# Performance work log

Hardware: AMD Instinct MI355X
Metric: run time of the kernel (lower is better)

Reference implementation:

```python
import jax, jax.numpy as jnp
import numpy as np

# ---- structural constants (mirror e3nn SO3.tensor_productRs bookkeeping) ----
MUL = 2                      # multiplicity of every irrep in Rs_in / Rs_out
LS = [0, 1, 2]               # irrep orders present in Rs_in and Rs_out
L_MAX = 2                    # spherical-harmonics cutoff -> Y_dim = 9
N_BASIS, HIDDEN = 64, 64     # radial model sizes
R_MAX, GAMMA = 3.5, 4.0      # gaussian radial basis params


def _filter_paths():
    """One entry (l_filter) per (mul_out, mul_in, l_in, l_out, l_f) path."""
    paths = []
    for l_in in LS:
        for l_out in LS:
            for lf in range(abs(l_in - l_out), min(l_in + l_out, L_MAX) + 1):
                paths.extend([lf] * (MUL * MUL))  # mul_in * mul_out copies
    return paths  # len == n_path == 60


def _build_mix_matrices():
    """rf_mix[K, n_path]: broadcast each radial path weight over its 2l+1 components.
    ylm_mix[K, 9]: select Y_{l,m} for each filter component. Both 0/1, block sparse."""
    paths = _filter_paths()
    n_path = len(paths)
    K = sum(2 * l + 1 for l in paths)          # 204
    y_off = {0: 0, 1: 1, 2: 4}                 # offset of l-block inside Y (dim 9)
    rf = np.zeros((K, n_path), dtype=np.float32)
    ylm = np.zeros((K, 9), dtype=np.float32)
    k = 0
    for p, l in enumerate(paths):
        for m in range(2 * l + 1):
            rf[k, p] = 1.0
            ylm[k, y_off[l] + m] = 1.0
            k += 1
    return rf, ylm, n_path, K


def _sh_l012(n):
    """Real spherical harmonics l=0..2 on unit vectors n[Z,3] -> Y[9, Z]."""
    x, y, z = n[:, 0], n[:, 1], n[:, 2]
    c0 = 0.28209479177387814   # 1/(2 sqrt(pi))
    c1 = 0.4886025119029199    # sqrt(3/(4 pi))
    c2a = 1.0925484305920792   # sqrt(15/(4 pi))
    c2b = 0.31539156525252005  # sqrt(5/(16 pi))
    c2c = 0.5462742152960396   # sqrt(15/(16 pi))
    one = jnp.ones_like(x)
    return jnp.stack([
        c0 * one,
        c1 * y, c1 * z, c1 * x,
        c2a * x * y, c2a * y * z, c2b * (3.0 * z * z - 1.0), c2a * x * z,
        c2c * (x * x - y * y),
    ], axis=0)


def setup_inputs() -> dict:
    key = jax.random.key(0)
    k_r, k_cg, k_w1, k_w2 = jax.random.split(key, 4)
    Z = 65536
    D = MUL * sum(2 * l + 1 for l in LS)       # 18 (dim_in == dim_out)
    rf_np, ylm_np, n_path, K = _build_mix_matrices()
    r = 2.0 * jax.random.normal(k_r, (Z, 3), dtype=jnp.float32)
    cg = jax.random.normal(k_cg, (K, D, D), dtype=jnp.float32) / np.sqrt(K)
    W1 = jax.random.normal(k_w1, (N_BASIS, HIDDEN), dtype=jnp.float32) / np.sqrt(N_BASIS)
    b1 = jnp.zeros((HIDDEN,), dtype=jnp.float32)
    W2 = jax.random.normal(k_w2, (HIDDEN, n_path), dtype=jnp.float32) / np.sqrt(HIDDEN)
    b2 = jnp.zeros((n_path,), dtype=jnp.float32)
    return {"r": r, "W1": W1, "b1": b1, "W2": W2, "b2": b2,
            "cg": cg, "rf_mix": jnp.asarray(rf_np), "ylm_mix": jnp.asarray(ylm_np)}


def reference(r, W1, b1, W2, b2, cg, rf_mix, ylm_mix):
    radii = jnp.linalg.norm(r, axis=1)                    # [Z]
    n = r / (radii[:, None] + 1e-12)                      # unit directions
    Y = _sh_l012(n)                                       # [9, Z]  (sh returns [m, ...])
    centers = jnp.linspace(0.0, R_MAX, N_BASIS, dtype=jnp.float32)
    B = jnp.exp(-GAMMA * (radii[:, None] - centers) ** 2) # gaussian radial basis [Z, 64]
    R = jax.nn.relu(B @ W1 + b1) @ W2 + b2                # RadialModel -> [Z, n_path]
    Rm = jnp.einsum('kp,zp->zk', rf_mix, R)               # 'ij,zj->zi'
    Ym = jnp.einsum('ky,yz->zk', ylm_mix, Y)              # 'ij,jz->zi'
    # 'kij,zk,zk->zij' : fuse the two per-point vectors, then one GEMM over k
    kernel = jnp.einsum('kij,zk->zij', cg, Rm * Ym)       # [Z, 18, 18]
    return kernel
```

## Files before the change

### kernel.cpp

```cpp
#include <hip/hip_runtime.h>

#define NPATH 60
#define KDIM  204
#define NIJ   324
#define NTIL  21
#define HID   64

typedef short bf16x8 __attribute__((ext_vector_type(8)));
typedef float f32x4  __attribute__((ext_vector_type(4)));

__device__ __align__(16) unsigned short g_w1s[4096];
__device__ __align__(16) unsigned short g_w2s[4096];
__device__ __align__(16) unsigned short g_cgs[75264];
__device__ unsigned int  g_pyk[112];

__device__ inline unsigned short f2bf(float f) {
    unsigned int u = __builtin_bit_cast(unsigned int, f);
    u += 0x7fffu + ((u >> 16) & 1u);
    return (unsigned short)(u >> 16);
}
__device__ inline float bf2f(unsigned short h) {
    unsigned int u = ((unsigned int)h) << 16;
    return __builtin_bit_cast(float, u);
}

__global__ void prep_kernel(const float* __restrict__ W1, const float* __restrict__ W2,
                            const float* __restrict__ cg, const float* __restrict__ rf,
                            const float* __restrict__ ylm)
{
    int idx = blockIdx.x * 256 + threadIdx.x;
    if (idx < 4096) {
        int e = idx & 7, ln = (idx >> 3) & 63, nt = (idx >> 9) & 3, kc = idx >> 11;
        int k = kc * 32 + (ln >> 4) * 8 + e;
        int n = nt * 16 + (ln & 15);
        g_w1s[idx] = f2bf(W1[k * HID + n]);
    } else if (idx < 8192) {
        int j = idx - 4096;
        int e = j & 7, ln = (j >> 3) & 63, nt = (j >> 9) & 3, kc = j >> 11;
        int k = kc * 32 + (ln >> 4) * 8 + e;
        int n = nt * 16 + (ln & 15);
        g_w2s[j] = f2bf(n < NPATH ? W2[k * NPATH + n] : 0.0f);
    } else if (idx < 8192 + 75264) {
        int j = idx - 8192;
        int e = j & 7, ln = (j >> 3) & 63;
        int nt = (j >> 9) % NTIL;
        int kc = j / (512 * NTIL);
        int k = kc * 32 + (ln >> 4) * 8 + e;
        int n = nt * 16 + (ln & 15);
        g_cgs[j] = f2bf((k < KDIM && n < NIJ) ? cg[k * NIJ + n] : 0.0f);
    } else if (idx < 8192 + 75264 + 112) {
        int j = idx - (8192 + 75264);
        int k0 = 2 * j, k1 = 2 * j + 1;
        unsigned p0 = 0, y0 = 0, p1 = 0, y1 = 0;
        if (k0 < KDIM) {
            for (int q = 0; q < NPATH; q++) if (rf[k0 * NPATH + q] != 0.0f) p0 = q;
            for (int q = 0; q < 9; q++)     if (ylm[k0 * 9 + q]   != 0.0f) y0 = q;
            for (int q = 0; q < NPATH; q++) if (rf[k1 * NPATH + q] != 0.0f) p1 = q;
            for (int q = 0; q < 9; q++)     if (ylm[k1 * 9 + q]   != 0.0f) y1 = q;
        }
        g_pyk[j] = p0 | (y0 << 8) | (p1 << 16) | (y1 << 24);
    }
}

struct __align__(16) WaveMem {
    unsigned short Hw[16][88];
    unsigned short Rw[16][61];
    float          Yw[16][9];
};

__global__ __launch_bounds__(256) void fused_kernel(
    const float* __restrict__ r, const float* __restrict__ b1,
    const float* __restrict__ b2, float* __restrict__ out)
{
    __shared__ WaveMem wm[4];

    const int tid  = threadIdx.x;
    const int wv   = tid >> 6;
    const int lane = tid & 63;
    const int quad = lane >> 4;
    const int l16  = lane & 15;
    const int z0   = blockIdx.x * 64;
    WaveMem& W = wm[wv];

    const int zg = z0 + wv * 16 + l16;
    float x = r[zg * 3 + 0], y = r[zg * 3 + 1], zc = r[zg * 3 + 2];
    float rad = sqrtf(x * x + y * y + zc * zc);

    if (quad == 0) {
        float inv = 1.0f / (rad + 1e-12f);
        float nx = x * inv, ny = y * inv, nz = zc * inv;
        const float c0 = 0.28209479177387814f, c1 = 0.4886025119029199f;
        const float c2a = 1.0925484305920792f, c2b = 0.31539156525252005f, c2c = 0.5462742152960396f;
        W.Yw[l16][0] = c0;
        W.Yw[l16][1] = c1 * ny;
        W.Yw[l16][2] = c1 * nz;
        W.Yw[l16][3] = c1 * nx;
        W.Yw[l16][4] = c2a * nx * ny;
        W.Yw[l16][5] = c2a * ny * nz;
        W.Yw[l16][6] = c2b * (3.0f * nz * nz - 1.0f);
        W.Yw[l16][7] = c2a * nx * nz;
        W.Yw[l16][8] = c2c * (nx * nx - ny * ny);
    }

    union frag { bf16x8 v; unsigned int d[4]; };
    frag A0, A1;
    {
        const float step = 3.5f / 63.0f;
        const float NL2E = -5.770780163555852f;
        #pragma unroll
        for (int ii = 0; ii < 4; ii++) {
            int i0 = quad * 8 + 2 * ii;
            float d0 = rad - (float)i0 * step;
            float d1 = rad - (float)(i0 + 1) * step;
            A0.d[ii] = (unsigned)f2bf(__builtin_amdgcn_exp2f(d0 * d0 * NL2E))
                     | ((unsigned)f2bf(__builtin_amdgcn_exp2f(d1 * d1 * NL2E)) << 16);
            int i2 = 32 + i0;
            float e0 = rad - (float)i2 * step;
            float e1 = rad - (float)(i2 + 1) * step;
            A1.d[ii] = (unsigned)f2bf(__builtin_amdgcn_exp2f(e0 * e0 * NL2E))
                     | ((unsigned)f2bf(__builtin_amdgcn_exp2f(e1 * e1 * NL2E)) << 16);
        }
    }

    #pragma unroll
    for (int nt = 0; nt < 4; nt++) {
        bf16x8 bb0 = *(const bf16x8*)&g_w1s[((0 * 4 + nt) * 64 + lane) * 8];
        bf16x8 bb1 = *(const bf16x8*)&g_w1s[((1 * 4 + nt) * 64 + lane) * 8];
        f32x4 acc = {0.f, 0.f, 0.f, 0.f};
        acc = __builtin_amdgcn_mfma_f32_16x16x32_bf16(A0.v, bb0, acc, 0, 0, 0);
        acc = __builtin_amdgcn_mfma_f32_16x16x32_bf16(A1.v, bb1, acc, 0, 0, 0);
        int h = nt * 16 + l16;
        float bias = b1[h];
        #pragma unroll
        for (int rr = 0; rr < 4; rr++) {
            float v = acc[rr] + bias;
            v = v > 0.0f ? v : 0.0f;
            W.Hw[quad * 4 + rr][h] = f2bf(v);
        }
    }
    asm volatile("s_waitcnt lgkmcnt(0)" ::: "memory");
    __builtin_amdgcn_sched_barrier(0);

    {
        bf16x8 h0 = *(const bf16x8*)&W.Hw[l16][0 + quad * 8];
        bf16x8 h1 = *(const bf16x8*)&W.Hw[l16][32 + quad * 8];
        #pragma unroll
        for (int nt = 0; nt < 4; nt++) {
            bf16x8 bb0 = *(const bf16x8*)&g_w2s[((0 * 4 + nt) * 64 + lane) * 8];
            bf16x8 bb1 = *(const bf16x8*)&g_w2s[((1 * 4 + nt) * 64 + lane) * 8];
            f32x4 acc = {0.f, 0.f, 0.f, 0.f};
            acc = __builtin_amdgcn_mfma_f32_16x16x32_bf16(h0, bb0, acc, 0, 0, 0);
            acc = __builtin_amdgcn_mfma_f32_16x16x32_bf16(h1, bb1, acc, 0, 0, 0);
            int p = nt * 16 + l16;
            if (p < NPATH) {
                float bias = b2[p];
                #pragma unroll
                for (int rr = 0; rr < 4; rr++)
                    W.Rw[quad * 4 + rr][p] = f2bf(acc[rr] + bias);
            }
        }
    }
    asm volatile("s_waitcnt lgkmcnt(0)" ::: "memory");
    __builtin_amdgcn_sched_barrier(0);

    frag az[7];
    #pragma unroll
    for (int kc = 0; kc < 7; kc++) {
        #pragma unroll
        for (int ii = 0; ii < 4; ii++) {
            unsigned py = g_pyk[kc * 16 + quad * 4 + ii];
            float cA = bf2f(W.Rw[l16][py & 255])         * W.Yw[l16][(py >> 8) & 255];
            float cB = bf2f(W.Rw[l16][(py >> 16) & 255]) * W.Yw[l16][py >> 24];
            az[kc].d[ii] = (unsigned)f2bf(cA) | ((unsigned)f2bf(cB) << 16);
        }
    }

    const int obase = (z0 + wv * 16 + quad * 4) * NIJ + l16;
    #pragma unroll 3
    for (int nt = 0; nt < NTIL; nt++) {
        f32x4 acc = {0.f, 0.f, 0.f, 0.f};
        #pragma unroll
        for (int kc = 0; kc < 7; kc++) {
            bf16x8 bg = *(const bf16x8*)&g_cgs[((kc * NTIL + nt) * 64 + lane) * 8];
            acc = __builtin_amdgcn_mfma_f32_16x16x32_bf16(az[kc].v, bg, acc, 0, 0, 0);
        }
        int col = nt * 16 + l16;
        if (col < NIJ) {
            #pragma unroll
            for (int rr = 0; rr < 4; rr++)
                out[obase + rr * NIJ + nt * 16] = acc[rr];
        }
    }
}

extern "C" void kernel_launch(void* const* d_in, const int* in_sizes, int n_in,
                              void* d_out, int out_size, void* d_ws, size_t ws_size,
                              hipStream_t stream) {
    const float* r   = (const float*)d_in[0];
    const float* W1  = (const float*)d_in[1];
    const float* b1  = (const float*)d_in[2];
    const float* W2  = (const float*)d_in[3];
    const float* b2  = (const float*)d_in[4];
    const float* cg  = (const float*)d_in[5];
    const float* rf  = (const float*)d_in[6];
    const float* ylm = (const float*)d_in[7];
    float* out = (float*)d_out;

    const int Z = in_sizes[0] / 3;

    prep_kernel<<<327, 256, 0, stream>>>(W1, W2, cg, rf, ylm);
    fused_kernel<<<Z / 64, 256, 0, stream>>>(r, b1, b2, out);
}
```

Measured before the change: 127.2 us.

## Process two 16-point tiles per wave to reuse CG fragments across MFMAs

Each wave now handles 32 points, running the radial MLP and coefficient phases twice into two A-fragment sets. In the final GEMM each loaded CG B-fragment feeds two MFMAs, halving CG loads per output and doubling the work per block (half as many blocks). The prep kernel's CG repack is also rewritten to iterate over source order so reads of cg are coalesced. The cost is more registers (two 7-fragment sets) and fewer blocks, which may reduce occupancy and latency hiding on the write-bound output stage.

```diff
diff --git a/kernel.cpp b/kernel.cpp
--- a/kernel.cpp
+++ b/kernel.cpp
@@ -42,12 +42,13 @@
         g_w2s[j] = f2bf(n < NPATH ? W2[k * NPATH + n] : 0.0f);
     } else if (idx < 8192 + 75264) {
         int j = idx - 8192;
-        int e = j & 7, ln = (j >> 3) & 63;
-        int nt = (j >> 9) % NTIL;
-        int kc = j / (512 * NTIL);
-        int k = kc * 32 + (ln >> 4) * 8 + e;
-        int n = nt * 16 + (ln & 15);
-        g_cgs[j] = f2bf((k < KDIM && n < NIJ) ? cg[k * NIJ + n] : 0.0f);
+        int k = j / 336;
+        int n = j % 336;
+        int kc = k >> 5, km = k & 31;
+        int e  = km & 7, lh = km >> 3;
+        int nt = n >> 4, lw = n & 15;
+        int dst = ((kc * NTIL + nt) * 64 + (lh * 16 + lw)) * 8 + e;
+        g_cgs[dst] = f2bf((k < KDIM && n < NIJ) ? cg[k * NIJ + n] : 0.0f);
     } else if (idx < 8192 + 75264 + 112) {
         int j = idx - (8192 + 75264);
         int k0 = 2 * j, k1 = 2 * j + 1;
@@ -68,6 +69,8 @@
     float          Yw[16][9];
 };
 
+union frag { bf16x8 v; unsigned int d[4]; };
+
 __global__ __launch_bounds__(256) void fused_kernel(
     const float* __restrict__ r, const float* __restrict__ b1,
     const float* __restrict__ b2, float* __restrict__ out)
@@ -79,116 +82,125 @@
     const int lane = tid & 63;
     const int quad = lane >> 4;
     const int l16  = lane & 15;
-    const int z0   = blockIdx.x * 64;
+    const int z0   = blockIdx.x * 128;
     WaveMem& W = wm[wv];
 
-    const int zg = z0 + wv * 16 + l16;
-    float x = r[zg * 3 + 0], y = r[zg * 3 + 1], zc = r[zg * 3 + 2];
-    float rad = sqrtf(x * x + y * y + zc * zc);
-
-    if (quad == 0) {
-        float inv = 1.0f / (rad + 1e-12f);
-        float nx = x * inv, ny = y * inv, nz = zc * inv;
-        const float c0 = 0.28209479177387814f, c1 = 0.4886025119029199f;
-        const float c2a = 1.0925484305920792f, c2b = 0.31539156525252005f, c2c = 0.5462742152960396f;
-        W.Yw[l16][0] = c0;
-        W.Yw[l16][1] = c1 * ny;
-        W.Yw[l16][2] = c1 * nz;
-        W.Yw[l16][3] = c1 * nx;
-        W.Yw[l16][4] = c2a * nx * ny;
-        W.Yw[l16][5] = c2a * ny * nz;
-        W.Yw[l16][6] = c2b * (3.0f * nz * nz - 1.0f);
-        W.Yw[l16][7] = c2a * nx * nz;
-        W.Yw[l16][8] = c2c * (nx * nx - ny * ny);
+    frag az0[7], az1[7];
+
+#define PHASES_AD(AZ, ZBASE)                                                          \
+    {                                                                                 \
+        const int zg = (ZBASE) + l16;                                                 \
+        float x = r[zg * 3 + 0], y = r[zg * 3 + 1], zc = r[zg * 3 + 2];               \
+        float rad = sqrtf(x * x + y * y + zc * zc);                                   \
+        if (quad == 0) {                                                              \
+            float inv = 1.0f / (rad + 1e-12f);                                        \
+            float nx = x * inv, ny = y * inv, nz = zc * inv;                          \
+            const float c0 = 0.28209479177387814f, c1 = 0.4886025119029199f;          \
+            const float c2a = 1.0925484305920792f, c2b = 0.31539156525252005f,        \
+                        c2c = 0.5462742152960396f;                                    \
+            W.Yw[l16][0] = c0;                                                        \
+            W.Yw[l16][1] = c1 * ny;                                                   \
+            W.Yw[l16][2] = c1 * nz;                                                   \
+            W.Yw[l16][3] = c1 * nx;                                                   \
+            W.Yw[l16][4] = c2a * nx * ny;                                             \
+            W.Yw[l16][5] = c2a * ny * nz;                                             \
+            W.Yw[l16][6] = c2b * (3.0f * nz * nz - 1.0f);                             \
+            W.Yw[l16][7] = c2a * nx * nz;                                             \
+            W.Yw[l16][8] = c2c * (nx * nx - ny * ny);                                 \
+        }                                                                             \
+        frag A0, A1;                                                                  \
+        {                                                                             \
+            const float step = 3.5f / 63.0f;                                          \
+            const float NL2E = -5.770780163555852f;                 \
+            _Pragma("unroll")                                                         \
+            for (int ii = 0; ii < 4; ii++) {                                          \
+                int i0 = quad * 8 + 2 * ii;                                           \
+                float d0 = rad - (float)i0 * step;                                    \
+                float d1 = rad - (float)(i0 + 1) * step;                              \
+                A0.d[ii] = (unsigned)f2bf(__builtin_amdgcn_exp2f(d0 * d0 * NL2E))     \
+                         | ((unsigned)f2bf(__builtin_amdgcn_exp2f(d1 * d1 * NL2E)) << 16); \
+                int i2 = 32 + i0;                                                     \
+                float e0 = rad - (float)i2 * step;                                    \
+                float e1 = rad - (float)(i2 + 1) * step;                              \
+                A1.d[ii] = (unsigned)f2bf(__builtin_amdgcn_exp2f(e0 * e0 * NL2E))     \
+                         | ((unsigned)f2bf(__builtin_amdgcn_exp2f(e1 * e1 * NL2E)) << 16); \
+            }                                                                         \
+        }                                                                             \
+        _Pragma("unroll")                                                             \
+        for (int nt = 0; nt < 4; nt++) {                                              \
+            bf16x8 bb0 = *(const bf16x8*)&g_w1s[((0 * 4 + nt) * 64 + lane) * 8];      \
+            bf16x8 bb1 = *(const bf16x8*)&g_w1s[((1 * 4 + nt) * 64 + lane) * 8];      \
+            f32x4 acc = {0.f, 0.f, 0.f, 0.f};                                         \
+            acc = __builtin_amdgcn_mfma_f32_16x16x32_bf16(A0.v, bb0, acc, 0, 0, 0);   \
+            acc = __builtin_amdgcn_mfma_f32_16x16x32_bf16(A1.v, bb1, acc, 0, 0, 0);   \
+            int h = nt * 16 + l16;                                                    \
+            float bias = b1[h];                                                       \
+            _Pragma("unroll")                                                         \
+            for (int rr = 0; rr < 4; rr++) {                                          \
+                float v = acc[rr] + bias;                                             \
+                v = v > 0.0f ? v : 0.0f;                                              \
+                W.Hw[quad * 4 + rr][h] = f2bf(v);                                     \
+            }                                                                         \
+        }                                                                             \
+        asm volatile("s_waitcnt lgkmcnt(0)" ::: "memory");                            \
+        __builtin_amdgcn_sched_barrier(0);                                            \
+        {                                                                             \
+            bf16x8 h0 = *(const bf16x8*)&W.Hw[l16][0 + quad * 8];                     \
+            bf16x8 h1 = *(const bf16x8*)&W.Hw[l16][32 + quad * 8];                    \
+            _Pragma("unroll")                                                         \
+            for (int nt = 0; nt < 4; nt++) {                                          \
+                bf16x8 bb0 = *(const bf16x8*)&g_w2s[((0 * 4 + nt) * 64 + lane) * 8];  \
+                bf16x8 bb1 = *(const bf16x8*)&g_w2s[((1 * 4 + nt) * 64 + lane) * 8];  \
+                f32x4 acc = {0.f, 0.f, 0.f, 0.f};                                     \
+                acc = __builtin_amdgcn_mfma_f32_16x16x32_bf16(h0, bb0, acc, 0, 0, 0); \
+                acc = __builtin_amdgcn_mfma_f32_16x16x32_bf16(h1, bb1, acc, 0, 0, 0); \
+                int p = nt * 16 + l16;                                                \
+                if (p < NPATH) {                                                      \
+                    float bias = b2[p];                                               \
+                    _Pragma("unroll")                                                 \
+                    for (int rr = 0; rr < 4; rr++)                                    \
+                        W.Rw[quad * 4 + rr][p] = f2bf(acc[rr] + bias);                \
+                }                                                                     \
+            }                                                                         \
+        }                                                                             \
+        asm volatile("s_waitcnt lgkmcnt(0)" ::: "memory");                            \
+        __builtin_amdgcn_sched_barrier(0);                                            \
+        _Pragma("unroll")                                                             \
+        for (int kc = 0; kc < 7; kc++) {                                              \
+            _Pragma("unroll")                                                         \
+            for (int ii = 0; ii < 4; ii++) {                                          \
+                unsigned py = g_pyk[kc * 16 + quad * 4 + ii];                         \
+                float cA = bf2f(W.Rw[l16][py & 255])         * W.Yw[l16][(py >> 8) & 255]; \
+                float cB = bf2f(W.Rw[l16][(py >> 16) & 255]) * W.Yw[l16][py >> 24];   \
+                AZ[kc].d[ii] = (unsigned)f2bf(cA) | ((unsigned)f2bf(cB) << 16);       \
+            }                                                                         \
+        }                                                                             \
+        asm volatile("s_waitcnt lgkmcnt(0)" ::: "memory");                            \
+        __builtin_amdgcn_sched_barrier(0);                                            \
     }
 
-    union frag { bf16x8 v; unsigned int d[4]; };
-    frag A0, A1;
-    {
-        const float step = 3.5f / 63.0f;
-        const float NL2E = -5.770780163555852f;
-        #pragma unroll
-        for (int ii = 0; ii < 4; ii++) {
-            int i0 = quad * 8 + 2 * ii;
-            float d0 = rad - (float)i0 * step;
-            float d1 = rad - (float)(i0 + 1) * step;
-            A0.d[ii] = (unsigned)f2bf(__builtin_amdgcn_exp2f(d0 * d0 * NL2E))
-                     | ((unsigned)f2bf(__builtin_amdgcn_exp2f(d1 * d1 * NL2E)) << 16);
-            int i2 = 32 + i0;
-            float e0 = rad - (float)i2 * step;
-            float e1 = rad - (float)(i2 + 1) * step;
-            A1.d[ii] = (unsigned)f2bf(__builtin_amdgcn_exp2f(e0 * e0 * NL2E))
-                     | ((unsigned)f2bf(__builtin_amdgcn_exp2f(e1 * e1 * NL2E)) << 16);
-        }
-    }
-
-    #pragma unroll
-    for (int nt = 0; nt < 4; nt++) {
-        bf16x8 bb0 = *(const bf16x8*)&g_w1s[((0 * 4 + nt) * 64 + lane) * 8];
-        bf16x8 bb1 = *(const bf16x8*)&g_w1s[((1 * 4 + nt) * 64 + lane) * 8];
-        f32x4 acc = {0.f, 0.f, 0.f, 0.f};
-        acc = __builtin_amdgcn_mfma_f32_16x16x32_bf16(A0.v, bb0, acc, 0, 0, 0);
-        acc = __builtin_amdgcn_mfma_f32_16x16x32_bf16(A1.v, bb1, acc, 0, 0, 0);
-        int h = nt * 16 + l16;
-        float bias = b1[h];
-        #pragma unroll
-        for (int rr = 0; rr < 4; rr++) {
-            float v = acc[rr] + bias;
-            v = v > 0.0f ? v : 0.0f;
-            W.Hw[quad * 4 + rr][h] = f2bf(v);
-        }
-    }
-    asm volatile("s_waitcnt lgkmcnt(0)" ::: "memory");
-    __builtin_amdgcn_sched_barrier(0);
-
-    {
-        bf16x8 h0 = *(const bf16x8*)&W.Hw[l16][0 + quad * 8];
-        bf16x8 h1 = *(const bf16x8*)&W.Hw[l16][32 + quad * 8];
-        #pragma unroll
-        for (int nt = 0; nt < 4; nt++) {
-            bf16x8 bb0 = *(const bf16x8*)&g_w2s[((0 * 4 + nt) * 64 + lane) * 8];
-            bf16x8 bb1 = *(const bf16x8*)&g_w2s[((1 * 4 + nt) * 64 + lane) * 8];
-            f32x4 acc = {0.f, 0.f, 0.f, 0.f};
-            acc = __builtin_amdgcn_mfma_f32_16x16x32_bf16(h0, bb0, acc, 0, 0, 0);
-            acc = __builtin_amdgcn_mfma_f32_16x16x32_bf16(h1, bb1, acc, 0, 0, 0);
-            int p = nt * 16 + l16;
-            if (p < NPATH) {
-                float bias = b2[p];
-                #pragma unroll
-                for (int rr = 0; rr < 4; rr++)
-                    W.Rw[quad * 4 + rr][p] = f2bf(acc[rr] + bias);
-            }
-        }
-    }
-    asm volatile("s_waitcnt lgkmcnt(0)" ::: "memory");
-    __builtin_amdgcn_sched_barrier(0);
-
-    frag az[7];
-    #pragma unroll
-    for (int kc = 0; kc < 7; kc++) {
-        #pragma unroll
-        for (int ii = 0; ii < 4; ii++) {
-            unsigned py = g_pyk[kc * 16 + quad * 4 + ii];
-            float cA = bf2f(W.Rw[l16][py & 255])         * W.Yw[l16][(py >> 8) & 255];
-            float cB = bf2f(W.Rw[l16][(py >> 16) & 255]) * W.Yw[l16][py >> 24];
-            az[kc].d[ii] = (unsigned)f2bf(cA) | ((unsigned)f2bf(cB) << 16);
-        }
-    }
-
-    const int obase = (z0 + wv * 16 + quad * 4) * NIJ + l16;
+    PHASES_AD(az0, z0 + wv * 32)
+    PHASES_AD(az1, z0 + wv * 32 + 16)
+#undef PHASES_AD
+
+    const int obase = (z0 + wv * 32 + quad * 4) * NIJ + l16;
     #pragma unroll 3
     for (int nt = 0; nt < NTIL; nt++) {
-        f32x4 acc = {0.f, 0.f, 0.f, 0.f};
+        f32x4 accA = {0.f, 0.f, 0.f, 0.f};
+        f32x4 accB = {0.f, 0.f, 0.f, 0.f};
         #pragma unroll
         for (int kc = 0; kc < 7; kc++) {
             bf16x8 bg = *(const bf16x8*)&g_cgs[((kc * NTIL + nt) * 64 + lane) * 8];
-            acc = __builtin_amdgcn_mfma_f32_16x16x32_bf16(az[kc].v, bg, acc, 0, 0, 0);
+            accA = __builtin_amdgcn_mfma_f32_16x16x32_bf16(az0[kc].v, bg, accA, 0, 0, 0);
+            accB = __builtin_amdgcn_mfma_f32_16x16x32_bf16(az1[kc].v, bg, accB, 0, 0, 0);
         }
         int col = nt * 16 + l16;
         if (col < NIJ) {
             #pragma unroll
-            for (int rr = 0; rr < 4; rr++)
-                out[obase + rr * NIJ + nt * 16] = acc[rr];
+            for (int rr = 0; rr < 4; rr++) {
+                out[obase + rr * NIJ + nt * 16]              = accA[rr];
+                out[obase + (16 + rr) * NIJ + nt * 16]       = accB[rr];
+            }
         }
     }
 }
@@ -209,5 +221,5 @@
     const int Z = in_sizes[0] / 3;
 
     prep_kernel<<<327, 256, 0, stream>>>(W1, W2, cg, rf, ylm);
-    fused_kernel<<<Z / 64, 256, 0, stream>>>(r, b1, b2, out);
-}
+    fused_kernel<<<Z / 128, 256, 0, stream>>>(r, b1, b2, out);
+}
```

Result: slower. 133.4 us (+4.9%).

## Split fused kernel into MLP and GEMM kernels via global coefficient buffer

Applied to the files above, without the earlier changes.

Splits the single fused kernel into an MLP kernel that writes per-point bf16 filter coefficients to a global buffer and a separate GEMM kernel that reads them and runs the CG contraction. The cg prep loop is also reindexed so global reads are coalesced while writes are scattered. The split lets each kernel get its own register and occupancy profile, but it adds a global round trip of about 29 MB and a second launch. The fixed ZMAX buffer caps Z at 65536.

```diff
diff --git a/kernel.cpp b/kernel.cpp
--- a/kernel.cpp
+++ b/kernel.cpp
@@ -5,6 +5,7 @@
 #define NIJ   324
 #define NTIL  21
 #define HID   64
+#define ZMAX  65536
 
 typedef short bf16x8 __attribute__((ext_vector_type(8)));
 typedef float f32x4  __attribute__((ext_vector_type(4)));
@@ -13,6 +14,7 @@
 __device__ __align__(16) unsigned short g_w2s[4096];
 __device__ __align__(16) unsigned short g_cgs[75264];
 __device__ unsigned int  g_pyk[112];
+__device__ __align__(16) unsigned short g_coef[ZMAX * 224];
 
 __device__ inline unsigned short f2bf(float f) {
     unsigned int u = __builtin_bit_cast(unsigned int, f);
@@ -42,12 +44,13 @@
         g_w2s[j] = f2bf(n < NPATH ? W2[k * NPATH + n] : 0.0f);
     } else if (idx < 8192 + 75264) {
         int j = idx - 8192;
-        int e = j & 7, ln = (j >> 3) & 63;
-        int nt = (j >> 9) % NTIL;
-        int kc = j / (512 * NTIL);
-        int k = kc * 32 + (ln >> 4) * 8 + e;
-        int n = nt * 16 + (ln & 15);
-        g_cgs[j] = f2bf((k < KDIM && n < NIJ) ? cg[k * NIJ + n] : 0.0f);
+        int k = j / 336;
+        int n = j % 336;
+        int kc = k >> 5, km = k & 31;
+        int e  = km & 7, lh = km >> 3;
+        int nt = n >> 4, lw = n & 15;
+        int dst = ((kc * NTIL + nt) * 64 + (lh * 16 + lw)) * 8 + e;
+        g_cgs[dst] = f2bf((k < KDIM && n < NIJ) ? cg[k * NIJ + n] : 0.0f);
     } else if (idx < 8192 + 75264 + 112) {
         int j = idx - (8192 + 75264);
         int k0 = 2 * j, k1 = 2 * j + 1;
@@ -68,9 +71,11 @@
     float          Yw[16][9];
 };
 
-__global__ __launch_bounds__(256) void fused_kernel(
+union frag { bf16x8 v; unsigned int d[4]; };
+
+__global__ __launch_bounds__(256) void mlp_kernel(
     const float* __restrict__ r, const float* __restrict__ b1,
-    const float* __restrict__ b2, float* __restrict__ out)
+    const float* __restrict__ b2)
 {
     __shared__ WaveMem wm[4];
 
@@ -102,7 +107,6 @@
         W.Yw[l16][8] = c2c * (nx * nx - ny * ny);
     }
 
-    union frag { bf16x8 v; unsigned int d[4]; };
     frag A0, A1;
     {
         const float step = 3.5f / 63.0f;
@@ -163,17 +167,34 @@
     asm volatile("s_waitcnt lgkmcnt(0)" ::: "memory");
     __builtin_amdgcn_sched_barrier(0);
 
-    frag az[7];
     #pragma unroll
     for (int kc = 0; kc < 7; kc++) {
+        frag az;
         #pragma unroll
         for (int ii = 0; ii < 4; ii++) {
             unsigned py = g_pyk[kc * 16 + quad * 4 + ii];
             float cA = bf2f(W.Rw[l16][py & 255])         * W.Yw[l16][(py >> 8) & 255];
             float cB = bf2f(W.Rw[l16][(py >> 16) & 255]) * W.Yw[l16][py >> 24];
-            az[kc].d[ii] = (unsigned)f2bf(cA) | ((unsigned)f2bf(cB) << 16);
-        }
-    }
+            az.d[ii] = (unsigned)f2bf(cA) | ((unsigned)f2bf(cB) << 16);
+        }
+        *(bf16x8*)&g_coef[zg * 224 + kc * 32 + quad * 8] = az.v;
+    }
+}
+
+__global__ __launch_bounds__(256) void gemm_kernel(float* __restrict__ out)
+{
+    const int tid  = threadIdx.x;
+    const int wv   = tid >> 6;
+    const int lane = tid & 63;
+    const int quad = lane >> 4;
+    const int l16  = lane & 15;
+    const int z0   = blockIdx.x * 64;
+
+    const int zrow = z0 + wv * 16 + l16;
+    frag az[7];
+    #pragma unroll
+    for (int kc = 0; kc < 7; kc++)
+        az[kc].v = *(const bf16x8*)&g_coef[zrow * 224 + kc * 32 + quad * 8];
 
     const int obase = (z0 + wv * 16 + quad * 4) * NIJ + l16;
     #pragma unroll 3
@@ -209,5 +230,6 @@
     const int Z = in_sizes[0] / 3;
 
     prep_kernel<<<327, 256, 0, stream>>>(W1, W2, cg, rf, ylm);
-    fused_kernel<<<Z / 64, 256, 0, stream>>>(r, b1, b2, out);
-}
+    mlp_kernel<<<Z / 64, 256, 0, stream>>>(r, b1, b2);
+    gemm_kernel<<<Z / 64, 256, 0, stream>>>(out);
+}
```

After: 138.4 us. 1.09x slower.

## Stage CG fragments through double-buffered shared memory shared across waves

Applied to the files above, without the earlier changes.

The CG B-fragments are now loaded cooperatively into a double-buffered LDS tile, with each wave fetching one or two k-chunks per output tile. All four waves then read the tile from shared memory instead of each fetching all seven chunks from global/L2. The prep kernel's CG swizzle is also reorganised so consecutive threads read contiguous source elements, making its global reads coalesced. The cost is a __syncthreads per output tile, which may stall waves, and an extra LDS write/read round trip.

```diff
diff --git a/kernel.cpp b/kernel.cpp
--- a/kernel.cpp
+++ b/kernel.cpp
@@ -42,12 +42,13 @@
         g_w2s[j] = f2bf(n < NPATH ? W2[k * NPATH + n] : 0.0f);
     } else if (idx < 8192 + 75264) {
         int j = idx - 8192;
-        int e = j & 7, ln = (j >> 3) & 63;
-        int nt = (j >> 9) % NTIL;
-        int kc = j / (512 * NTIL);
-        int k = kc * 32 + (ln >> 4) * 8 + e;
-        int n = nt * 16 + (ln & 15);
-        g_cgs[j] = f2bf((k < KDIM && n < NIJ) ? cg[k * NIJ + n] : 0.0f);
+        int k = j / 336;
+        int n = j % 336;
+        int kc = k >> 5, km = k & 31;
+        int e  = km & 7, lh = km >> 3;
+        int nt = n >> 4, lw = n & 15;
+        int dst = ((kc * NTIL + nt) * 64 + (lh * 16 + lw)) * 8 + e;
+        g_cgs[dst] = f2bf((k < KDIM && n < NIJ) ? cg[k * NIJ + n] : 0.0f);
     } else if (idx < 8192 + 75264 + 112) {
         int j = idx - (8192 + 75264);
         int k0 = 2 * j, k1 = 2 * j + 1;
@@ -68,11 +69,14 @@
     float          Yw[16][9];
 };
 
+union frag { bf16x8 v; unsigned int d[4]; };
+
 __global__ __launch_bounds__(256) void fused_kernel(
     const float* __restrict__ r, const float* __restrict__ b1,
     const float* __restrict__ b2, float* __restrict__ out)
 {
     __shared__ WaveMem wm[4];
+    __shared__ __align__(16) unsigned short CgBuf[2][7][512];
 
     const int tid  = threadIdx.x;
     const int wv   = tid >> 6;
@@ -102,7 +106,6 @@
         W.Yw[l16][8] = c2c * (nx * nx - ny * ny);
     }
 
-    union frag { bf16x8 v; unsigned int d[4]; };
     frag A0, A1;
     {
         const float step = 3.5f / 63.0f;
@@ -176,14 +179,38 @@
     }
 
     const int obase = (z0 + wv * 16 + quad * 4) * NIJ + l16;
-    #pragma unroll 3
+
+    {
+        bf16x8 s0 = *(const bf16x8*)&g_cgs[((wv * NTIL + 0) * 64 + lane) * 8];
+        bf16x8 s1 = {};
+        if (wv < 3) s1 = *(const bf16x8*)&g_cgs[(((wv + 4) * NTIL + 0) * 64 + lane) * 8];
+        *(bf16x8*)&CgBuf[0][wv][lane * 8] = s0;
+        if (wv < 3) *(bf16x8*)&CgBuf[0][wv + 4][lane * 8] = s1;
+    }
+    __syncthreads();
+
     for (int nt = 0; nt < NTIL; nt++) {
+        const int buf = nt & 1;
+
+        bf16x8 s0 = {}, s1 = {};
+        if (nt + 1 < NTIL) {
+            s0 = *(const bf16x8*)&g_cgs[((wv * NTIL + nt + 1) * 64 + lane) * 8];
+            if (wv < 3) s1 = *(const bf16x8*)&g_cgs[(((wv + 4) * NTIL + nt + 1) * 64 + lane) * 8];
+        }
+
         f32x4 acc = {0.f, 0.f, 0.f, 0.f};
         #pragma unroll
         for (int kc = 0; kc < 7; kc++) {
-            bf16x8 bg = *(const bf16x8*)&g_cgs[((kc * NTIL + nt) * 64 + lane) * 8];
+            bf16x8 bg = *(const bf16x8*)&CgBuf[buf][kc][lane * 8];
             acc = __builtin_amdgcn_mfma_f32_16x16x32_bf16(az[kc].v, bg, acc, 0, 0, 0);
         }
+
+        if (nt + 1 < NTIL) {
+            *(bf16x8*)&CgBuf[buf ^ 1][wv][lane * 8] = s0;
+            if (wv < 3) *(bf16x8*)&CgBuf[buf ^ 1][wv + 4][lane * 8] = s1;
+            __syncthreads();
+        }
+
         int col = nt * 16 + l16;
         if (col < NIJ) {
             #pragma unroll
```

New measurement: 130.8 us. 1.03x slower.
